# Performance work log

Hardware: AMD Instinct MI355X
Metric: run time of the kernel (lower is better)

The kernel has to match this reference:

```python
import jax, jax.numpy as jnp
import numpy as np

NEG_SLOPE = 0.2  # PyG GATv2Conv default negative_slope


def gatv2_layer(x, src, dst, edge_attr, Wl, bl, Wr, br, We, att, bias):
    # Faithful PyG GATv2Conv (heads=H, concat=True, edge_dim=1, add_self_loops=True,
    # fill_value='mean', share_weights=False).
    N = x.shape[0]
    H, C = att.shape
    xl = (x @ Wl + bl).reshape(N, H, C)  # source-side transform (x_j)
    xr = (x @ Wr + br).reshape(N, H, C)  # target-side transform (x_i)
    valid = src != dst  # PyG removes pre-existing self loops before adding its own
    w = valid.astype(x.dtype)[:, None]
    # self-loop edge_attr = per-dst mean of incoming (non-self-loop) edge_attr
    sums = jax.ops.segment_sum(edge_attr * w, dst, num_segments=N)
    cnts = jax.ops.segment_sum(w, dst, num_segments=N)
    loop_attr = jnp.where(cnts > 0, sums / jnp.maximum(cnts, 1.0), 0.0)  # [N,1]
    e = (edge_attr @ We).reshape(-1, H, C)      # lin_edge (bias=False)  [E,H,C]
    e_loop = (loop_attr @ We).reshape(N, H, C)  # [N,H,C]
    # GATv2 scoring: leaky_relu(x_i + x_j + e) . att
    m = jax.nn.leaky_relu(xl[src] + xr[dst] + e, NEG_SLOPE)      # [E,H,C]
    score = jnp.where(valid[:, None], (m * att).sum(-1), -jnp.inf)  # [E,H]
    m_loop = jax.nn.leaky_relu(xl + xr + e_loop, NEG_SLOPE)      # [N,H,C]
    score_loop = (m_loop * att).sum(-1)                          # [N,H]
    # segment softmax over incoming edges + self loop, per dst node
    smax = jnp.maximum(jax.ops.segment_max(score, dst, num_segments=N), score_loop)
    ex = jnp.where(valid[:, None], jnp.exp(score - smax[dst]), 0.0)
    ex_loop = jnp.exp(score_loop - smax)
    denom = jax.ops.segment_sum(ex, dst, num_segments=N) + ex_loop  # [N,H]
    alpha = ex / denom[dst]
    alpha_loop = ex_loop / denom
    # aggregate alpha * x_j (transformed source features)
    out = jax.ops.segment_sum(alpha[..., None] * xl[src], dst, num_segments=N)
    out = out + alpha_loop[..., None] * xl
    return out.reshape(N, H * C) + bias


def setup_inputs() -> dict:
    key = jax.random.key(0)
    ks = jax.random.split(key, 16)
    N, E, D_IN, HID, H, D_OUT = 20000, 640000, 128, 32, 4, 64
    HC = H * HID  # 128
    s = lambda fan_in: 1.0 / np.sqrt(fan_in)
    inp = {
        "x": jax.random.normal(ks[0], (N, D_IN), jnp.float32),
        "edge_index": jax.random.randint(ks[1], (2, E), 0, N, jnp.int64),
        "edge_attr": jax.random.normal(ks[2], (E, 1), jnp.float32),
        "Wl1": jax.random.normal(ks[3], (D_IN, HC), jnp.float32) * s(D_IN),
        "bl1": jnp.zeros((HC,), jnp.float32),
        "Wr1": jax.random.normal(ks[4], (D_IN, HC), jnp.float32) * s(D_IN),
        "br1": jnp.zeros((HC,), jnp.float32),
        "We1": jax.random.normal(ks[5], (1, HC), jnp.float32),
        "att1": jax.random.normal(ks[6], (H, HID), jnp.float32) * s(HID),
        "b1": jnp.zeros((HC,), jnp.float32),
        "Wl2": jax.random.normal(ks[7], (HC, HC), jnp.float32) * s(HC),
        "bl2": jnp.zeros((HC,), jnp.float32),
        "Wr2": jax.random.normal(ks[8], (HC, HC), jnp.float32) * s(HC),
        "br2": jnp.zeros((HC,), jnp.float32),
        "We2": jax.random.normal(ks[9], (1, HC), jnp.float32),
        "att2": jax.random.normal(ks[10], (H, HID), jnp.float32) * s(HID),
        "b2": jnp.zeros((HC,), jnp.float32),
        "Wo": jax.random.normal(ks[11], (HC, D_OUT), jnp.float32) * s(HC),
        "bo": jnp.zeros((D_OUT,), jnp.float32),
    }
    return inp


def reference(x, edge_index, edge_attr, Wl1, bl1, Wr1, br1, We1, att1, b1,
              Wl2, bl2, Wr2, br2, We2, att2, b2, Wo, bo):
    src, dst = edge_index[0], edge_index[1]
    h = jax.nn.elu(gatv2_layer(x, src, dst, edge_attr, Wl1, bl1, Wr1, br1, We1, att1, b1))
    h = jax.nn.elu(gatv2_layer(h, src, dst, edge_attr, Wl2, bl2, Wr2, br2, We2, att2, b2))
    return h @ Wo + bo
```

## Files before the change

### kernel.cpp

```cpp
#include <hip/hip_runtime.h>
#include <math.h>


#define CHUNK 32


__global__ void hist_rank_kernel(const int* __restrict__ ei, int E,
                                 int* __restrict__ deg, int* __restrict__ rank) {
    int e = blockIdx.x * blockDim.x + threadIdx.x;
    if (e < E) {
        int s = ei[e], d = ei[E + e];
        if (s != d)
            rank[e] = atomicAdd(&deg[d], 1);
    }
}

__global__ __launch_bounds__(1024) void scan_kernel(const int* __restrict__ deg,
                                                    int* __restrict__ rowptr, int N) {
    __shared__ int wsum[16];
    const int t = threadIdx.x;
    const int lane = t & 63, wid = t >> 6;
    const int base = t * CHUNK;
    int loc[CHUNK];
    int s = 0;
#pragma unroll
    for (int j = 0; j < CHUNK; ++j) {
        int idx = base + j;
        int v = (idx < N) ? deg[idx] : 0;
        loc[j] = s;
        s += v;
    }
    int sc = s;
#pragma unroll
    for (int off = 1; off < 64; off <<= 1) {
        int y = __shfl_up(sc, off);
        if (lane >= off) sc += y;
    }
    if (lane == 63) wsum[wid] = sc;
    __syncthreads();
    if (wid == 0) {
        int w = (lane < 16) ? wsum[lane] : 0;
#pragma unroll
        for (int off = 1; off < 16; off <<= 1) {
            int y = __shfl_up(w, off);
            if (lane >= off) w += y;
        }
        if (lane < 16) wsum[lane] = w;
    }
    __syncthreads();
    const int woff = (wid > 0) ? wsum[wid - 1] : 0;
    const int texcl = woff + sc - s;
#pragma unroll
    for (int j = 0; j < CHUNK; ++j) {
        int idx = base + j;
        if (idx < N) rowptr[idx] = texcl + loc[j];
    }
    if (t == 1023) rowptr[N] = wsum[15];
}

__global__ void scatter_kernel(const int* __restrict__ ei, const float* __restrict__ ea,
                               const int* __restrict__ rank,
                               const int* __restrict__ rowptr,
                               int2* __restrict__ csr, int E) {
    int e = blockIdx.x * blockDim.x + threadIdx.x;
    if (e < E) {
        int s = ei[e], d = ei[E + e];
        if (s != d) {
            int pos = rowptr[d] + rank[e];
            csr[pos] = make_int2(s, __float_as_int(ea[e]));
        }
    }
}


#define FMA_ROW(accrow, aval, bvec)                                            \
    accrow[0] = fmaf(aval, bvec.x, accrow[0]);                                 \
    accrow[1] = fmaf(aval, bvec.y, accrow[1]);                                 \
    accrow[2] = fmaf(aval, bvec.z, accrow[2]);                                 \
    accrow[3] = fmaf(aval, bvec.w, accrow[3]);

__global__ __launch_bounds__(256) void gemm_tile(const float* __restrict__ A,
                                                 const float* __restrict__ B,
                                                 const float* __restrict__ bias,
                                                 float* __restrict__ C,
                                                 int M, int NCOL) {
    __shared__ float As[64 * 132];
    __shared__ float Bs[128 * 64];
    const int tid = threadIdx.x;
    const int tx = tid & 15, ty = tid >> 4;
    const int row0 = blockIdx.x * 64;
    const int col0 = blockIdx.y * 64;

#pragma unroll
    for (int it = 0; it < 8; ++it) {
        int i = tid * 4 + it * 1024;
        int r = i >> 7, k0 = i & 127;
        int gr = row0 + r;
        float4 v = make_float4(0.f, 0.f, 0.f, 0.f);
        if (gr < M) v = *(const float4*)&A[(size_t)gr * 128 + k0];
        *(float4*)&As[r * 132 + k0] = v;
    }
#pragma unroll
    for (int it = 0; it < 8; ++it) {
        int i = tid * 4 + it * 1024;
        int k = i >> 6, cc = i & 63;
        *(float4*)&Bs[k * 64 + cc] = *(const float4*)&B[(size_t)k * NCOL + col0 + cc];
    }
    __syncthreads();

    float acc[4][4];
#pragma unroll
    for (int r = 0; r < 4; ++r)
        acc[r][0] = acc[r][1] = acc[r][2] = acc[r][3] = 0.f;

    const int bcol = 4 * tx;
    const int arow = 4 * ty;
#pragma unroll 2
    for (int k0 = 0; k0 < 128; k0 += 4) {
        float4 a0 = *(const float4*)&As[(arow + 0) * 132 + k0];
        float4 a1 = *(const float4*)&As[(arow + 1) * 132 + k0];
        float4 a2 = *(const float4*)&As[(arow + 2) * 132 + k0];
        float4 a3 = *(const float4*)&As[(arow + 3) * 132 + k0];
        float4 b0 = *(const float4*)&Bs[(k0 + 0) * 64 + bcol];
        float4 b1 = *(const float4*)&Bs[(k0 + 1) * 64 + bcol];
        float4 b2 = *(const float4*)&Bs[(k0 + 2) * 64 + bcol];
        float4 b3 = *(const float4*)&Bs[(k0 + 3) * 64 + bcol];
        FMA_ROW(acc[0], a0.x, b0) FMA_ROW(acc[1], a1.x, b0)
        FMA_ROW(acc[2], a2.x, b0) FMA_ROW(acc[3], a3.x, b0)
        FMA_ROW(acc[0], a0.y, b1) FMA_ROW(acc[1], a1.y, b1)
        FMA_ROW(acc[2], a2.y, b1) FMA_ROW(acc[3], a3.y, b1)
        FMA_ROW(acc[0], a0.z, b2) FMA_ROW(acc[1], a1.z, b2)
        FMA_ROW(acc[2], a2.z, b2) FMA_ROW(acc[3], a3.z, b2)
        FMA_ROW(acc[0], a0.w, b3) FMA_ROW(acc[1], a1.w, b3)
        FMA_ROW(acc[2], a2.w, b3) FMA_ROW(acc[3], a3.w, b3)
    }

    float4 bv = *(const float4*)&bias[col0 + bcol];
#pragma unroll
    for (int rr = 0; rr < 4; ++rr) {
        int gr = row0 + arow + rr;
        if (gr < M) {
            float4 o = make_float4(acc[rr][0] + bv.x, acc[rr][1] + bv.y,
                                   acc[rr][2] + bv.z, acc[rr][3] + bv.w);
            *(float4*)&C[(size_t)gr * NCOL + col0 + bcol] = o;
        }
    }
}


__device__ __forceinline__ void gat_update(float xlx, float xly, float a,
                                           float xrx, float xry,
                                           float wex, float wey,
                                           float atx, float aty,
                                           float& m, float& den,
                                           float& acc0, float& acc1) {
    float t0 = fmaf(a, wex, xlx + xrx);
    float t1 = fmaf(a, wey, xly + xry);
    t0 = fmaxf(t0, 0.2f * t0);
    t1 = fmaxf(t1, 0.2f * t1);
    float sc = fmaf(t0, atx, t1 * aty);
    sc += __shfl_xor(sc, 1);
    sc += __shfl_xor(sc, 2);
    sc += __shfl_xor(sc, 4);
    sc += __shfl_xor(sc, 8);
    float mn = fmaxf(m, sc);
    float rr = __expf(m - mn);
    float pw = __expf(sc - mn);
    den = fmaf(den, rr, pw);
    acc0 = fmaf(acc0, rr, pw * xlx);
    acc1 = fmaf(acc1, rr, pw * xly);
    m = mn;
}

#define GAT_BATCH 16

__global__ __launch_bounds__(256, 4) void gat_fused(
    const float* __restrict__ xl, const float* __restrict__ xr,
    const int2* __restrict__ csr,
    const float* __restrict__ We, const float* __restrict__ att,
    const float* __restrict__ bias, const int* __restrict__ rowptr,
    float* __restrict__ out, int N) {
    const int node = (blockIdx.x * blockDim.x + threadIdx.x) >> 6;
    const int lane = threadIdx.x & 63;
    if (node >= N) return;
    const int c = lane * 2;

    const float2 xrv = *(const float2*)&xr[(size_t)node * 128 + c];
    const float2 wev = *(const float2*)&We[c];
    const float2 atv = *(const float2*)&att[c];

    float m = -INFINITY, den = 0.f, acc0 = 0.f, acc1 = 0.f;
    float easum = 0.f;
    const int beg = __builtin_amdgcn_readfirstlane(rowptr[node]);
    const int end = __builtin_amdgcn_readfirstlane(rowptr[node + 1]);

    int p = beg;
    for (; p + GAT_BATCH <= end; p += GAT_BATCH) {
        int2 cv[GAT_BATCH]; float2 xv[GAT_BATCH];
#pragma unroll
        for (int j = 0; j < GAT_BATCH; ++j) cv[j] = csr[p + j];
#pragma unroll
        for (int j = 0; j < GAT_BATCH; ++j)
            xv[j] = *(const float2*)&xl[(size_t)cv[j].x * 128 + c];
#pragma unroll
        for (int j = 0; j < GAT_BATCH; ++j) {
            float a = __int_as_float(cv[j].y);
            easum += a;
            gat_update(xv[j].x, xv[j].y, a, xrv.x, xrv.y, wev.x, wev.y,
                       atv.x, atv.y, m, den, acc0, acc1);
        }
    }
    if (p < end) {
        int2 cv[GAT_BATCH]; float2 xv[GAT_BATCH];
#pragma unroll
        for (int j = 0; j < GAT_BATCH; ++j) {
            int q = (p + j < end) ? (p + j) : p;
            cv[j] = csr[q];
        }
#pragma unroll
        for (int j = 0; j < GAT_BATCH; ++j)
            xv[j] = *(const float2*)&xl[(size_t)cv[j].x * 128 + c];
#pragma unroll
        for (int j = 0; j < GAT_BATCH; ++j)
            if (p + j < end) {
                float a = __int_as_float(cv[j].y);
                easum += a;
                gat_update(xv[j].x, xv[j].y, a, xrv.x, xrv.y, wev.x, wev.y,
                           atv.x, atv.y, m, den, acc0, acc1);
            }
    }

    const int degn = end - beg;
    const float al = (degn > 0) ? easum / (float)degn : 0.f;
    const float2 xself = *(const float2*)&xl[(size_t)node * 128 + c];
    gat_update(xself.x, xself.y, al, xrv.x, xrv.y, wev.x, wev.y,
               atv.x, atv.y, m, den, acc0, acc1);

    const float inv = 1.f / den;
    float o0 = acc0 * inv + bias[c];
    float o1 = acc1 * inv + bias[c + 1];
    o0 = o0 > 0.f ? o0 : __expf(o0) - 1.f;
    o1 = o1 > 0.f ? o1 : __expf(o1) - 1.f;
    *(float2*)&out[(size_t)node * 128 + c] = make_float2(o0, o1);
}


extern "C" void kernel_launch(void* const* d_in, const int* in_sizes, int n_in,
                              void* d_out, int out_size, void* d_ws, size_t ws_size,
                              hipStream_t stream) {
    const float* x    = (const float*)d_in[0];
    const int*   ei   = (const int*)d_in[1];
    const float* ea   = (const float*)d_in[2];
    const float* Wl1  = (const float*)d_in[3];
    const float* bl1  = (const float*)d_in[4];
    const float* Wr1  = (const float*)d_in[5];
    const float* br1  = (const float*)d_in[6];
    const float* We1  = (const float*)d_in[7];
    const float* att1 = (const float*)d_in[8];
    const float* b1   = (const float*)d_in[9];
    const float* Wl2  = (const float*)d_in[10];
    const float* bl2  = (const float*)d_in[11];
    const float* Wr2  = (const float*)d_in[12];
    const float* br2  = (const float*)d_in[13];
    const float* We2  = (const float*)d_in[14];
    const float* att2 = (const float*)d_in[15];
    const float* b2   = (const float*)d_in[16];
    const float* Wo   = (const float*)d_in[17];
    const float* bo   = (const float*)d_in[18];
    float* out = (float*)d_out;

    const int N = in_sizes[0] / 128;
    const int E = in_sizes[1] / 2;

    char* base = (char*)d_ws;
    size_t off = 0;
    auto alloc = [&](size_t bytes) -> void* {
        void* p = base + off;
        off += (bytes + 255) & ~(size_t)255;
        return p;
    };
    float* xl      = (float*)alloc((size_t)N * 128 * 4);
    float* xr      = (float*)alloc((size_t)N * 128 * 4);
    float* h       = (float*)alloc((size_t)N * 128 * 4);
    int*   deg     = (int*)alloc((size_t)N * 4);
    int*   rowptr  = (int*)alloc(((size_t)N + 1) * 4);
    int*   rank    = (int*)alloc((size_t)E * 4);
    int2*  csr     = (int2*)alloc((size_t)E * 8);

    hipMemsetAsync(deg, 0, (size_t)N * 4, stream);
    hist_rank_kernel<<<(E + 255) / 256, 256, 0, stream>>>(ei, E, deg, rank);
    scan_kernel<<<1, 1024, 0, stream>>>(deg, rowptr, N);
    scatter_kernel<<<(E + 255) / 256, 256, 0, stream>>>(ei, ea, rank, rowptr, csr, E);

    const dim3 g2(( (unsigned)(N + 63) / 64 ), 2);
    const dim3 g1(( (unsigned)(N + 63) / 64 ), 1);
    const int fblk = (N + 3) / 4;

    gemm_tile<<<g2, 256, 0, stream>>>(x, Wl1, bl1, xl, N, 128);
    gemm_tile<<<g2, 256, 0, stream>>>(x, Wr1, br1, xr, N, 128);
    gat_fused<<<fblk, 256, 0, stream>>>(xl, xr, csr, We1, att1, b1, rowptr, h, N);

    gemm_tile<<<g2, 256, 0, stream>>>(h, Wl2, bl2, xl, N, 128);
    gemm_tile<<<g2, 256, 0, stream>>>(h, Wr2, br2, xr, N, 128);
    gat_fused<<<fblk, 256, 0, stream>>>(xl, xr, csr, We2, att2, b2, rowptr, h, N);

    gemm_tile<<<g1, 256, 0, stream>>>(h, Wo, bo, out, N, 64);
}
```

Baseline: 340.1 us.

## Fuse dual GEMMs, split GAT edges across two waves, use DPP reductions

Merges the Wl and Wr projections into one GEMM kernel that stages the A tile once and reuses it for both weight matrices, with B staged in two 64-row halves to cut shared memory. The GAT aggregation now splits each node's edge list across two wavefronts and merges their online-softmax partial states through shared memory, doubling the wave parallelism per node. The score reduction switches from shfl_xor to DPP row-rotate adds, and the online-softmax update computes a single exp instead of two. Costs are an extra __syncthreads, a shared-memory merge per node, and half the waves idling during the final epilogue.

```diff
diff --git a/kernel.cpp b/kernel.cpp
--- a/kernel.cpp
+++ b/kernel.cpp
@@ -79,13 +79,15 @@
     accrow[2] = fmaf(aval, bvec.z, accrow[2]);                                 \
     accrow[3] = fmaf(aval, bvec.w, accrow[3]);
 
-__global__ __launch_bounds__(256) void gemm_tile(const float* __restrict__ A,
-                                                 const float* __restrict__ B,
-                                                 const float* __restrict__ bias,
-                                                 float* __restrict__ C,
-                                                 int M, int NCOL) {
+__global__ __launch_bounds__(256) void gemm_dual(
+    const float* __restrict__ A,
+    const float* __restrict__ B0, const float* __restrict__ bias0,
+    float* __restrict__ C0,
+    const float* __restrict__ B1, const float* __restrict__ bias1,
+    float* __restrict__ C1,
+    int M, int NCOL) {
     __shared__ float As[64 * 132];
-    __shared__ float Bs[128 * 64];
+    __shared__ float Bs[64 * 64];
     const int tid = threadIdx.x;
     const int tx = tid & 15, ty = tid >> 4;
     const int row0 = blockIdx.x * 64;
@@ -100,53 +102,72 @@
         if (gr < M) v = *(const float4*)&A[(size_t)gr * 128 + k0];
         *(float4*)&As[r * 132 + k0] = v;
     }
-#pragma unroll
-    for (int it = 0; it < 8; ++it) {
-        int i = tid * 4 + it * 1024;
-        int k = i >> 6, cc = i & 63;
-        *(float4*)&Bs[k * 64 + cc] = *(const float4*)&B[(size_t)k * NCOL + col0 + cc];
-    }
-    __syncthreads();
-
-    float acc[4][4];
-#pragma unroll
-    for (int r = 0; r < 4; ++r)
-        acc[r][0] = acc[r][1] = acc[r][2] = acc[r][3] = 0.f;
 
     const int bcol = 4 * tx;
     const int arow = 4 * ty;
-#pragma unroll 2
-    for (int k0 = 0; k0 < 128; k0 += 4) {
-        float4 a0 = *(const float4*)&As[(arow + 0) * 132 + k0];
-        float4 a1 = *(const float4*)&As[(arow + 1) * 132 + k0];
-        float4 a2 = *(const float4*)&As[(arow + 2) * 132 + k0];
-        float4 a3 = *(const float4*)&As[(arow + 3) * 132 + k0];
-        float4 b0 = *(const float4*)&Bs[(k0 + 0) * 64 + bcol];
-        float4 b1 = *(const float4*)&Bs[(k0 + 1) * 64 + bcol];
-        float4 b2 = *(const float4*)&Bs[(k0 + 2) * 64 + bcol];
-        float4 b3 = *(const float4*)&Bs[(k0 + 3) * 64 + bcol];
-        FMA_ROW(acc[0], a0.x, b0) FMA_ROW(acc[1], a1.x, b0)
-        FMA_ROW(acc[2], a2.x, b0) FMA_ROW(acc[3], a3.x, b0)
-        FMA_ROW(acc[0], a0.y, b1) FMA_ROW(acc[1], a1.y, b1)
-        FMA_ROW(acc[2], a2.y, b1) FMA_ROW(acc[3], a3.y, b1)
-        FMA_ROW(acc[0], a0.z, b2) FMA_ROW(acc[1], a1.z, b2)
-        FMA_ROW(acc[2], a2.z, b2) FMA_ROW(acc[3], a3.z, b2)
-        FMA_ROW(acc[0], a0.w, b3) FMA_ROW(acc[1], a1.w, b3)
-        FMA_ROW(acc[2], a2.w, b3) FMA_ROW(acc[3], a3.w, b3)
-    }
-
-    float4 bv = *(const float4*)&bias[col0 + bcol];
-#pragma unroll
-    for (int rr = 0; rr < 4; ++rr) {
-        int gr = row0 + arow + rr;
-        if (gr < M) {
-            float4 o = make_float4(acc[rr][0] + bv.x, acc[rr][1] + bv.y,
-                                   acc[rr][2] + bv.z, acc[rr][3] + bv.w);
-            *(float4*)&C[(size_t)gr * NCOL + col0 + bcol] = o;
-        }
-    }
-}
-
+
+    for (int mi = 0; mi < 2; ++mi) {
+        const float* B = mi ? B1 : B0;
+        if (!B) break;
+        const float* bias = mi ? bias1 : bias0;
+        float* C = mi ? C1 : C0;
+
+        float acc[4][4];
+#pragma unroll
+        for (int r = 0; r < 4; ++r)
+            acc[r][0] = acc[r][1] = acc[r][2] = acc[r][3] = 0.f;
+
+        for (int kh = 0; kh < 128; kh += 64) {
+            __syncthreads();
+#pragma unroll
+            for (int it = 0; it < 4; ++it) {
+                int i = tid * 4 + it * 1024;
+                int k = i >> 6, cc = i & 63;
+                *(float4*)&Bs[k * 64 + cc] =
+                    *(const float4*)&B[(size_t)(kh + k) * NCOL + col0 + cc];
+            }
+            __syncthreads();
+
+#pragma unroll 4
+            for (int kk = 0; kk < 64; kk += 4) {
+                float4 a0 = *(const float4*)&As[(arow + 0) * 132 + kh + kk];
+                float4 a1 = *(const float4*)&As[(arow + 1) * 132 + kh + kk];
+                float4 a2 = *(const float4*)&As[(arow + 2) * 132 + kh + kk];
+                float4 a3 = *(const float4*)&As[(arow + 3) * 132 + kh + kk];
+                float4 b0 = *(const float4*)&Bs[(kk + 0) * 64 + bcol];
+                float4 b1 = *(const float4*)&Bs[(kk + 1) * 64 + bcol];
+                float4 b2 = *(const float4*)&Bs[(kk + 2) * 64 + bcol];
+                float4 b3 = *(const float4*)&Bs[(kk + 3) * 64 + bcol];
+                FMA_ROW(acc[0], a0.x, b0) FMA_ROW(acc[1], a1.x, b0)
+                FMA_ROW(acc[2], a2.x, b0) FMA_ROW(acc[3], a3.x, b0)
+                FMA_ROW(acc[0], a0.y, b1) FMA_ROW(acc[1], a1.y, b1)
+                FMA_ROW(acc[2], a2.y, b1) FMA_ROW(acc[3], a3.y, b1)
+                FMA_ROW(acc[0], a0.z, b2) FMA_ROW(acc[1], a1.z, b2)
+                FMA_ROW(acc[2], a2.z, b2) FMA_ROW(acc[3], a3.z, b2)
+                FMA_ROW(acc[0], a0.w, b3) FMA_ROW(acc[1], a1.w, b3)
+                FMA_ROW(acc[2], a2.w, b3) FMA_ROW(acc[3], a3.w, b3)
+            }
+        }
+
+        float4 bv = *(const float4*)&bias[col0 + bcol];
+#pragma unroll
+        for (int rr = 0; rr < 4; ++rr) {
+            int gr = row0 + arow + rr;
+            if (gr < M) {
+                float4 o = make_float4(acc[rr][0] + bv.x, acc[rr][1] + bv.y,
+                                       acc[rr][2] + bv.z, acc[rr][3] + bv.w);
+                *(float4*)&C[(size_t)gr * NCOL + col0 + bcol] = o;
+            }
+        }
+    }
+}
+
+
+template <int ROR>
+__device__ __forceinline__ float dpp_ror_add(float x) {
+    int y = __builtin_amdgcn_update_dpp(0, __float_as_int(x), 0x120 + ROR, 0xf, 0xf, true);
+    return x + __int_as_float(y);
+}
 
 __device__ __forceinline__ void gat_update(float xlx, float xly, float a,
                                            float xrx, float xry,
@@ -159,20 +180,22 @@
     t0 = fmaxf(t0, 0.2f * t0);
     t1 = fmaxf(t1, 0.2f * t1);
     float sc = fmaf(t0, atx, t1 * aty);
-    sc += __shfl_xor(sc, 1);
-    sc += __shfl_xor(sc, 2);
-    sc += __shfl_xor(sc, 4);
-    sc += __shfl_xor(sc, 8);
-    float mn = fmaxf(m, sc);
-    float rr = __expf(m - mn);
-    float pw = __expf(sc - mn);
+    sc = dpp_ror_add<1>(sc);
+    sc = dpp_ror_add<2>(sc);
+    sc = dpp_ror_add<4>(sc);
+    sc = dpp_ror_add<8>(sc);
+    float d = sc - m;
+    float e = __expf(-fabsf(d));
+    bool up = d > 0.f;
+    float rr = up ? e : 1.f;
+    float pw = up ? 1.f : e;
+    m = up ? sc : m;
     den = fmaf(den, rr, pw);
     acc0 = fmaf(acc0, rr, pw * xlx);
     acc1 = fmaf(acc1, rr, pw * xly);
-    m = mn;
-}
-
-#define GAT_BATCH 16
+}
+
+#define GB 16
 
 __global__ __launch_bounds__(256, 4) void gat_fused(
     const float* __restrict__ xl, const float* __restrict__ xr,
@@ -180,49 +203,57 @@
     const float* __restrict__ We, const float* __restrict__ att,
     const float* __restrict__ bias, const int* __restrict__ rowptr,
     float* __restrict__ out, int N) {
-    const int node = (blockIdx.x * blockDim.x + threadIdx.x) >> 6;
+    __shared__ float4 part[4][64];
+    __shared__ float esums[4];
+    const int wid = threadIdx.x >> 6;
     const int lane = threadIdx.x & 63;
-    if (node >= N) return;
+    const int w = wid & 1;
+    const int node = blockIdx.x * 2 + (wid >> 1);
     const int c = lane * 2;
 
-    const float2 xrv = *(const float2*)&xr[(size_t)node * 128 + c];
-    const float2 wev = *(const float2*)&We[c];
-    const float2 atv = *(const float2*)&att[c];
-
-    float m = -INFINITY, den = 0.f, acc0 = 0.f, acc1 = 0.f;
-    float easum = 0.f;
-    const int beg = __builtin_amdgcn_readfirstlane(rowptr[node]);
-    const int end = __builtin_amdgcn_readfirstlane(rowptr[node + 1]);
-
-    int p = beg;
-    for (; p + GAT_BATCH <= end; p += GAT_BATCH) {
-        int2 cv[GAT_BATCH]; float2 xv[GAT_BATCH];
-#pragma unroll
-        for (int j = 0; j < GAT_BATCH; ++j) cv[j] = csr[p + j];
-#pragma unroll
-        for (int j = 0; j < GAT_BATCH; ++j)
+    float m = -INFINITY, den = 0.f, acc0 = 0.f, acc1 = 0.f, easum = 0.f;
+    float2 xrv = make_float2(0.f, 0.f), wev = xrv, atv = xrv;
+    int beg = 0, end = 0, b0 = 0, e0 = 0;
+    if (node < N) {
+        xrv = *(const float2*)&xr[(size_t)node * 128 + c];
+        wev = *(const float2*)&We[c];
+        atv = *(const float2*)&att[c];
+        beg = __builtin_amdgcn_readfirstlane(rowptr[node]);
+        end = __builtin_amdgcn_readfirstlane(rowptr[node + 1]);
+        const int mid = beg + ((end - beg) >> 1);
+        b0 = w ? mid : beg;
+        e0 = w ? end : mid;
+    }
+
+    int p = b0;
+    for (; p + GB <= e0; p += GB) {
+        int2 cv[GB]; float2 xv[GB];
+#pragma unroll
+        for (int j = 0; j < GB; ++j) cv[j] = csr[p + j];
+#pragma unroll
+        for (int j = 0; j < GB; ++j)
             xv[j] = *(const float2*)&xl[(size_t)cv[j].x * 128 + c];
 #pragma unroll
-        for (int j = 0; j < GAT_BATCH; ++j) {
+        for (int j = 0; j < GB; ++j) {
             float a = __int_as_float(cv[j].y);
             easum += a;
             gat_update(xv[j].x, xv[j].y, a, xrv.x, xrv.y, wev.x, wev.y,
                        atv.x, atv.y, m, den, acc0, acc1);
         }
     }
-    if (p < end) {
-        int2 cv[GAT_BATCH]; float2 xv[GAT_BATCH];
-#pragma unroll
-        for (int j = 0; j < GAT_BATCH; ++j) {
-            int q = (p + j < end) ? (p + j) : p;
+    if (p < e0) {
+        int2 cv[GB]; float2 xv[GB];
+#pragma unroll
+        for (int j = 0; j < GB; ++j) {
+            int q = (p + j < e0) ? (p + j) : p;
             cv[j] = csr[q];
         }
 #pragma unroll
-        for (int j = 0; j < GAT_BATCH; ++j)
+        for (int j = 0; j < GB; ++j)
             xv[j] = *(const float2*)&xl[(size_t)cv[j].x * 128 + c];
 #pragma unroll
-        for (int j = 0; j < GAT_BATCH; ++j)
-            if (p + j < end) {
+        for (int j = 0; j < GB; ++j)
+            if (p + j < e0) {
                 float a = __int_as_float(cv[j].y);
                 easum += a;
                 gat_update(xv[j].x, xv[j].y, a, xrv.x, xrv.y, wev.x, wev.y,
@@ -230,18 +261,35 @@
             }
     }
 
-    const int degn = end - beg;
-    const float al = (degn > 0) ? easum / (float)degn : 0.f;
-    const float2 xself = *(const float2*)&xl[(size_t)node * 128 + c];
-    gat_update(xself.x, xself.y, al, xrv.x, xrv.y, wev.x, wev.y,
-               atv.x, atv.y, m, den, acc0, acc1);
-
-    const float inv = 1.f / den;
-    float o0 = acc0 * inv + bias[c];
-    float o1 = acc1 * inv + bias[c + 1];
-    o0 = o0 > 0.f ? o0 : __expf(o0) - 1.f;
-    o1 = o1 > 0.f ? o1 : __expf(o1) - 1.f;
-    *(float2*)&out[(size_t)node * 128 + c] = make_float2(o0, o1);
+    part[wid][lane] = make_float4(m, den, acc0, acc1);
+    if (lane == 0) esums[wid] = easum;
+    __syncthreads();
+
+    if (w == 0 && node < N) {
+        float4 p0 = part[wid][lane];
+        float4 p1 = part[wid + 1][lane];
+        float mn = fmaxf(p0.x, p1.x);
+        float e0f = (p0.x == mn) ? 1.f : __expf(p0.x - mn);
+        float e1f = (p1.x == mn) ? 1.f : __expf(p1.x - mn);
+        m = mn;
+        den = p0.y * e0f + p1.y * e1f;
+        acc0 = p0.z * e0f + p1.z * e1f;
+        acc1 = p0.w * e0f + p1.w * e1f;
+        easum = esums[wid] + esums[wid + 1];
+
+        const int degn = end - beg;
+        const float al = (degn > 0) ? easum / (float)degn : 0.f;
+        const float2 xself = *(const float2*)&xl[(size_t)node * 128 + c];
+        gat_update(xself.x, xself.y, al, xrv.x, xrv.y, wev.x, wev.y,
+                   atv.x, atv.y, m, den, acc0, acc1);
+
+        const float inv = 1.f / den;
+        float o0 = acc0 * inv + bias[c];
+        float o1 = acc1 * inv + bias[c + 1];
+        o0 = o0 > 0.f ? o0 : __expf(o0) - 1.f;
+        o1 = o1 > 0.f ? o1 : __expf(o1) - 1.f;
+        *(float2*)&out[(size_t)node * 128 + c] = make_float2(o0, o1);
+    }
 }
 
 
@@ -292,17 +340,15 @@
     scan_kernel<<<1, 1024, 0, stream>>>(deg, rowptr, N);
     scatter_kernel<<<(E + 255) / 256, 256, 0, stream>>>(ei, ea, rank, rowptr, csr, E);
 
-    const dim3 g2(( (unsigned)(N + 63) / 64 ), 2);
-    const dim3 g1(( (unsigned)(N + 63) / 64 ), 1);
-    const int fblk = (N + 3) / 4;
-
-    gemm_tile<<<g2, 256, 0, stream>>>(x, Wl1, bl1, xl, N, 128);
-    gemm_tile<<<g2, 256, 0, stream>>>(x, Wr1, br1, xr, N, 128);
+    const dim3 g2((unsigned)(N + 63) / 64, 2);
+    const dim3 g1((unsigned)(N + 63) / 64, 1);
+    const int fblk = (N + 1) / 2;
+
+    gemm_dual<<<g2, 256, 0, stream>>>(x, Wl1, bl1, xl, Wr1, br1, xr, N, 128);
     gat_fused<<<fblk, 256, 0, stream>>>(xl, xr, csr, We1, att1, b1, rowptr, h, N);
 
-    gemm_tile<<<g2, 256, 0, stream>>>(h, Wl2, bl2, xl, N, 128);
-    gemm_tile<<<g2, 256, 0, stream>>>(h, Wr2, br2, xr, N, 128);
+    gemm_dual<<<g2, 256, 0, stream>>>(h, Wl2, bl2, xl, Wr2, br2, xr, N, 128);
     gat_fused<<<fblk, 256, 0, stream>>>(xl, xr, csr, We2, att2, b2, rowptr, h, N);
 
-    gemm_tile<<<g1, 256, 0, stream>>>(h, Wo, bo, out, N, 64);
-}
+    gemm_dual<<<g1, 256, 0, stream>>>(h, Wo, bo, out, nullptr, nullptr, nullptr, N, 64);
+}
```

Measured after the change: 352.1 us. 3.5% more time.
